# Performance work log

Hardware: AMD Instinct MI355X
Metric: run time of the kernel (lower is better)

## Reference

```python
import jax, jax.numpy as jnp
import numpy as np

WS = 32          # window_size -> N = WS*WS = 1024
DIM = 1024
HEADS = 16
BATCH = 16


def _local_mask():
    # token i maps to grid cell (i//WS, i%WS); attend iff within 3x3 neighborhood
    idx = jnp.arange(WS * WS)
    r, c = idx // WS, idx % WS
    return (jnp.abs(r[:, None] - r[None, :]) <= 1) & (jnp.abs(c[:, None] - c[None, :]) <= 1)


def setup_inputs() -> dict:
    key = jax.random.key(0)
    k1, k2, k3 = jax.random.split(key, 3)
    N = WS * WS
    x = jax.random.normal(k1, (BATCH, N, DIM), dtype=jnp.float32)
    w_qkv = jax.random.normal(k2, (3 * DIM, DIM), dtype=jnp.float32) * 0.02
    w_proj = jax.random.normal(k3, (DIM, DIM), dtype=jnp.float32) * 0.02
    b_proj = jnp.zeros((DIM,), dtype=jnp.float32)
    return {"x": x, "w_qkv": w_qkv, "w_proj": w_proj, "b_proj": b_proj}


def reference(x, w_qkv, w_proj, b_proj):
    B, N, C = x.shape
    H = HEADS
    D = C // H
    scale = D ** (-0.5)
    # qkv projection: torch Linear is x @ W^T
    qkv = (x @ w_qkv.T).reshape(B, N, 3, H, D).transpose(2, 0, 3, 1, 4)  # (3,B,H,N,D)
    q, k, v = qkv[0], qkv[1], qkv[2]
    attn = jnp.einsum('bhnd,bhmd->bhnm', q, k) * scale  # (B,H,N,N)
    mask = _local_mask()  # (N,N) bool
    attn = jnp.where(mask[None, None], attn, -jnp.inf)
    attn = jax.nn.softmax(attn, axis=-1)
    out = jnp.einsum('bhnm,bhmd->bhnd', attn, v)          # (B,H,N,D)
    out = out.transpose(0, 2, 1, 3).reshape(B, N, C)      # (B,N,C)
    return out @ w_proj.T + b_proj
```

## Files before the change

### kernel.cpp

```cpp
#include <hip/hip_runtime.h>
#include <hip/hip_bf16.h>
#include <stdint.h>


typedef __bf16 bf16;
typedef __bf16 bf16x4_t __attribute__((ext_vector_type(4)));
typedef __bf16 bf16x8_t __attribute__((ext_vector_type(8)));
typedef float f32x4_t __attribute__((ext_vector_type(4)));

static __device__ __forceinline__ void gload_lds16(const void* g, void* l) {
  __builtin_amdgcn_global_load_lds((__attribute__((address_space(1))) void*)g,
                                   (__attribute__((address_space(3))) void*)l,
                                   16, 0, 0);
}

static __device__ __forceinline__ void block_barrier() {
  asm volatile("" ::: "memory");
  __builtin_amdgcn_s_barrier();
  asm volatile("" ::: "memory");
}

__global__ void cvt_all(const float* __restrict__ x, const float* __restrict__ wq,
                        const float* __restrict__ wp, bf16* __restrict__ xb,
                        bf16* __restrict__ wqb, bf16* __restrict__ wpb) {
  constexpr int NX = 4194304, NWQ = 786432;
  int i = blockIdx.x * blockDim.x + threadIdx.x;
  const float* src; bf16* dst; int off;
  if (i < NX)            { src = x;  dst = xb;  off = i; }
  else if (i < NX + NWQ) { src = wq; dst = wqb; off = i - NX; }
  else                   { src = wp; dst = wpb; off = i - (NX + NWQ); }
  float4 v = reinterpret_cast<const float4*>(src)[off];
  bf16x4_t o;
  o[0] = (bf16)v.x; o[1] = (bf16)v.y; o[2] = (bf16)v.z; o[3] = (bf16)v.w;
  reinterpret_cast<bf16x4_t*>(dst)[off] = o;
}

template<int OUT_BF16>
__global__ __launch_bounds__(512, 2)
void gemm3s(const bf16* __restrict__ A, const bf16* __restrict__ Bm,
            void* __restrict__ Cout, const float* __restrict__ bias,
            int M, int N, int K) {
  constexpr int SLOT = 32768;
  extern __shared__ __align__(16) char lds[];

  const int tid = threadIdx.x;
  const int w = tid >> 6, lane = tid & 63;
  const int fr = lane & 15, g = lane >> 4;
  const int wr = w >> 2, wc = w & 3;

  const int nwg = gridDim.x * gridDim.y;
  int lid = blockIdx.y * gridDim.x + blockIdx.x;
  lid = (lid & 7) * (nwg >> 3) + (lid >> 3);
  const int bx = lid % gridDim.x, by = lid / gridDim.x;
  const int row0 = by * 256, col0 = bx * 256;

  const bf16* Ag = A + (size_t)row0 * K;
  const bf16* Bg = Bm + (size_t)col0 * K;
  const int srow = tid >> 2;
  const int scol = ((tid & 3) ^ ((tid >> 3) & 3)) * 8;
  const int nkt  = K >> 5;

  f32x4_t acc[8][4] = {};

  auto stage = [&](int kt, int slot) {
    const int kb = kt << 5;
    char* sb = lds + slot * SLOT;
    gload_lds16(Ag + (size_t)(srow) * K + kb + scol,       sb + tid * 16);
    gload_lds16(Ag + (size_t)(128 + srow) * K + kb + scol, sb + 8192 + tid * 16);
    gload_lds16(Bg + (size_t)(srow) * K + kb + scol,       sb + 16384 + tid * 16);
    gload_lds16(Bg + (size_t)(128 + srow) * K + kb + scol, sb + 24576 + tid * 16);
  };

  const int uxor = ((fr >> 1) & 3) << 4;

  stage(0, 0);
  stage(1, 1);
  asm volatile("s_waitcnt vmcnt(4)" ::: "memory");
  block_barrier();

  int sl = 0;
  for (int kt = 0; kt < nkt; ++kt) {
    const bool pf = (kt + 2 < nkt);
    int s2 = sl + 2; if (s2 >= 3) s2 -= 3;
    if (pf) stage(kt + 2, s2);
    const char* cA = lds + sl * SLOT;
    const char* cB = cA + 16384;

    bf16x8_t a0[4], a1[4], b0[2], b1[2];
    auto lda = [&](bf16x8_t (&dst)[4], int q) {
#pragma unroll
      for (int i = 0; i < 4; ++i) {
        const int row = wr * 128 + (q * 4 + i) * 16 + fr;
        dst[i] = *reinterpret_cast<const bf16x8_t*>(cA + (row << 6) + ((g << 4) ^ uxor));
      }
    };
    auto ldb = [&](bf16x8_t (&dst)[2], int q) {
#pragma unroll
      for (int j = 0; j < 2; ++j) {
        const int row = wc * 64 + (q * 2 + j) * 16 + fr;
        dst[j] = *reinterpret_cast<const bf16x8_t*>(cB + (row << 6) + ((g << 4) ^ uxor));
      }
    };

    lda(a0, 0);
    ldb(b0, 0);
#pragma unroll
    for (int i = 0; i < 4; ++i)
#pragma unroll
      for (int j = 0; j < 2; ++j)
        acc[i][j] = __builtin_amdgcn_mfma_f32_16x16x32_bf16(a0[i], b0[j], acc[i][j], 0, 0, 0);
    ldb(b1, 1);
#pragma unroll
    for (int i = 0; i < 4; ++i)
#pragma unroll
      for (int j = 0; j < 2; ++j)
        acc[i][2 + j] = __builtin_amdgcn_mfma_f32_16x16x32_bf16(a0[i], b1[j], acc[i][2 + j], 0, 0, 0);
    lda(a1, 1);
#pragma unroll
    for (int i = 0; i < 4; ++i)
#pragma unroll
      for (int j = 0; j < 2; ++j)
        acc[4 + i][2 + j] = __builtin_amdgcn_mfma_f32_16x16x32_bf16(
            a1[i], b1[j], acc[4 + i][2 + j], 0, 0, 0);
#pragma unroll
    for (int i = 0; i < 4; ++i)
#pragma unroll
      for (int j = 0; j < 2; ++j)
        acc[4 + i][j] = __builtin_amdgcn_mfma_f32_16x16x32_bf16(
            a1[i], b0[j], acc[4 + i][j], 0, 0, 0);

    if (pf) asm volatile("s_waitcnt vmcnt(4)" ::: "memory");
    else    asm volatile("s_waitcnt vmcnt(0)" ::: "memory");
    block_barrier();
    sl = (sl + 1 == 3) ? 0 : sl + 1;
  }

#pragma unroll
  for (int fm = 0; fm < 8; ++fm) {
    const int rbase = row0 + wr * 128 + fm * 16 + g * 4;
#pragma unroll
    for (int fn = 0; fn < 4; ++fn) {
      const int col = col0 + wc * 64 + fn * 16 + fr;
#pragma unroll
      for (int r = 0; r < 4; ++r) {
        const size_t idx = (size_t)(rbase + r) * N + col;
        if constexpr (OUT_BF16) {
          reinterpret_cast<bf16*>(Cout)[idx] = (bf16)acc[fm][fn][r];
        } else {
          reinterpret_cast<float*>(Cout)[idx] = acc[fm][fn][r] + bias[col];
        }
      }
    }
  }
}

__global__ __launch_bounds__(256)
void local_attn(const bf16* __restrict__ qkv, bf16* __restrict__ outp) {
  const int tid  = threadIdx.x;
  const int wave = tid >> 6, lane = tid & 63;
  const int tsub = lane >> 3, ch = lane & 7;
  const int gt = (blockIdx.x * 4 + wave) * 8 + tsub;
  const int i  = gt & 1023;
  const int bh = gt >> 10;
  const int h  = bh & 15, b = bh >> 4;
  const int r  = i >> 5, c = i & 31;

  const bf16* base = qkv + (size_t)(b * 1024) * 3072 + h * 64 + ch * 8;

  bf16x8_t qv = *reinterpret_cast<const bf16x8_t*>(base + (size_t)i * 3072);
  float qf[8];
#pragma unroll
  for (int e = 0; e < 8; ++e) qf[e] = (float)qv[e];

  int jj[9]; float inval[9];
#pragma unroll
  for (int t = 0; t < 9; ++t) {
    const int dr = t / 3 - 1, dc = t % 3 - 1;
    const int rr = r + dr, cc = c + dc;
    const int rcl = min(max(rr, 0), 31), ccl = min(max(cc, 0), 31);
    jj[t] = rcl * 32 + ccl;
    inval[t] = (rr == rcl && cc == ccl) ? 0.f : -1e30f;
  }

  bf16x8_t kv[9], vv[9];
#pragma unroll
  for (int t = 0; t < 9; ++t)
    kv[t] = *reinterpret_cast<const bf16x8_t*>(base + (size_t)jj[t] * 3072 + 1024);
#pragma unroll
  for (int t = 0; t < 9; ++t)
    vv[t] = *reinterpret_cast<const bf16x8_t*>(base + (size_t)jj[t] * 3072 + 2048);

  float s[9];
#pragma unroll
  for (int t = 0; t < 9; ++t) {
    float ps = 0.f;
#pragma unroll
    for (int e = 0; e < 8; ++e) ps += qf[e] * (float)kv[t][e];
    ps += __shfl_xor(ps, 1);
    ps += __shfl_xor(ps, 2);
    ps += __shfl_xor(ps, 4);
    s[t] = ps * 0.125f + inval[t];
  }

  float mx = s[0];
#pragma unroll
  for (int t = 1; t < 9; ++t) mx = fmaxf(mx, s[t]);

  float denom = 0.f, o[8] = {};
#pragma unroll
  for (int t = 0; t < 9; ++t) {
    const float p = __expf(s[t] - mx);
    denom += p;
#pragma unroll
    for (int e = 0; e < 8; ++e) o[e] += p * (float)vv[t][e];
  }

  const float inv = 1.f / denom;
  bf16x8_t ov;
#pragma unroll
  for (int e = 0; e < 8; ++e) ov[e] = (bf16)(o[e] * inv);
  *reinterpret_cast<bf16x8_t*>(outp + (size_t)(b * 1024 + i) * 1024 + h * 64 + ch * 8) = ov;
}

extern "C" void kernel_launch(void* const* d_in, const int* in_sizes, int n_in,
                              void* d_out, int out_size, void* d_ws, size_t ws_size,
                              hipStream_t stream) {
  const float* x      = (const float*)d_in[0];
  const float* w_qkv  = (const float*)d_in[1];
  const float* w_proj = (const float*)d_in[2];
  const float* b_proj = (const float*)d_in[3];
  float* out = (float*)d_out;

  const size_t nx   = (size_t)16384 * 1024;
  const size_t nwq  = (size_t)3072 * 1024;
  const size_t nwp  = (size_t)1024 * 1024;
  const size_t nqkv = (size_t)16384 * 3072;

  bf16* x_bf  = (bf16*)d_ws;
  bf16* wq_bf = x_bf + nx;
  bf16* wp_bf = wq_bf + nwq;
  bf16* qkv   = wp_bf + nwp;
  bf16* attn  = qkv + nqkv;

  (void)hipFuncSetAttribute((const void*)&gemm3s<1>,
                            hipFuncAttributeMaxDynamicSharedMemorySize, 98304);
  (void)hipFuncSetAttribute((const void*)&gemm3s<0>,
                            hipFuncAttributeMaxDynamicSharedMemorySize, 98304);

  cvt_all<<<20480, 256, 0, stream>>>(x, w_qkv, w_proj, x_bf, wq_bf, wp_bf);

  gemm3s<1><<<dim3(3072 / 256, 16384 / 256), 512, 98304, stream>>>(
      x_bf, wq_bf, qkv, nullptr, 16384, 3072, 1024);

  local_attn<<<8192, 256, 0, stream>>>(qkv, attn);

  gemm3s<0><<<dim3(1024 / 256, 16384 / 256), 512, 98304, stream>>>(
      attn, wp_bf, out, b_proj, 16384, 1024, 1024);
}
```

Baseline: 213.0 us.

## Shrink GEMM tile to 256x128 with 4 waves and stage attention K/V rows in LDS

The GEMM drops from 256x256 tiles with 8 waves to 256x128 tiles with 4 waves, which shrinks LDS per stage and doubles the number of workgroups. The goal is better occupancy and load balance across CUs. The local attention kernel now maps one block to one (batch, head, row). It loads the three neighbouring K/V token rows into LDS once, so each token no longer issues 9 separate global gathers. In exchange, each GEMM tile reuses less data, and the attention kernel adds a barrier and LDS traffic.

```diff
diff --git a/kernel.cpp b/kernel.cpp
--- a/kernel.cpp
+++ b/kernel.cpp
@@ -36,23 +36,23 @@
 }
 
 template<int OUT_BF16>
-__global__ __launch_bounds__(512, 2)
-void gemm3s(const bf16* __restrict__ A, const bf16* __restrict__ Bm,
+__global__ __launch_bounds__(256, 2)
+void gemm4w(const bf16* __restrict__ A, const bf16* __restrict__ Bm,
             void* __restrict__ Cout, const float* __restrict__ bias,
             int M, int N, int K) {
-  constexpr int SLOT = 32768;
+  constexpr int SLOT = 24576;
   extern __shared__ __align__(16) char lds[];
 
   const int tid = threadIdx.x;
   const int w = tid >> 6, lane = tid & 63;
   const int fr = lane & 15, g = lane >> 4;
-  const int wr = w >> 2, wc = w & 3;
+  const int wr = w >> 1, wc = w & 1;
 
   const int nwg = gridDim.x * gridDim.y;
   int lid = blockIdx.y * gridDim.x + blockIdx.x;
   lid = (lid & 7) * (nwg >> 3) + (lid >> 3);
   const int bx = lid % gridDim.x, by = lid / gridDim.x;
-  const int row0 = by * 256, col0 = bx * 256;
+  const int row0 = by * 256, col0 = bx * 128;
 
   const bf16* Ag = A + (size_t)row0 * K;
   const bf16* Bg = Bm + (size_t)col0 * K;
@@ -65,17 +65,21 @@
   auto stage = [&](int kt, int slot) {
     const int kb = kt << 5;
     char* sb = lds + slot * SLOT;
-    gload_lds16(Ag + (size_t)(srow) * K + kb + scol,       sb + tid * 16);
-    gload_lds16(Ag + (size_t)(128 + srow) * K + kb + scol, sb + 8192 + tid * 16);
-    gload_lds16(Bg + (size_t)(srow) * K + kb + scol,       sb + 16384 + tid * 16);
-    gload_lds16(Bg + (size_t)(128 + srow) * K + kb + scol, sb + 24576 + tid * 16);
+#pragma unroll
+    for (int n = 0; n < 4; ++n)
+      gload_lds16(Ag + (size_t)(n * 64 + srow) * K + kb + scol,
+                  sb + n * 4096 + tid * 16);
+#pragma unroll
+    for (int n = 0; n < 2; ++n)
+      gload_lds16(Bg + (size_t)(n * 64 + srow) * K + kb + scol,
+                  sb + 16384 + n * 4096 + tid * 16);
   };
 
   const int uxor = ((fr >> 1) & 3) << 4;
 
   stage(0, 0);
   stage(1, 1);
-  asm volatile("s_waitcnt vmcnt(4)" ::: "memory");
+  asm volatile("s_waitcnt vmcnt(6)" ::: "memory");
   block_barrier();
 
   int sl = 0;
@@ -129,7 +133,7 @@
         acc[4 + i][j] = __builtin_amdgcn_mfma_f32_16x16x32_bf16(
             a1[i], b0[j], acc[4 + i][j], 0, 0, 0);
 
-    if (pf) asm volatile("s_waitcnt vmcnt(4)" ::: "memory");
+    if (pf) asm volatile("s_waitcnt vmcnt(6)" ::: "memory");
     else    asm volatile("s_waitcnt vmcnt(0)" ::: "memory");
     block_barrier();
     sl = (sl + 1 == 3) ? 0 : sl + 1;
@@ -156,50 +160,55 @@
 
 __global__ __launch_bounds__(256)
 void local_attn(const bf16* __restrict__ qkv, bf16* __restrict__ outp) {
+  __shared__ __align__(16) char sK[12288];
+  __shared__ __align__(16) char sV[12288];
+
   const int tid  = threadIdx.x;
-  const int wave = tid >> 6, lane = tid & 63;
-  const int tsub = lane >> 3, ch = lane & 7;
-  const int gt = (blockIdx.x * 4 + wave) * 8 + tsub;
-  const int i  = gt & 1023;
-  const int bh = gt >> 10;
-  const int h  = bh & 15, b = bh >> 4;
-  const int r  = i >> 5, c = i & 31;
-
-  const bf16* base = qkv + (size_t)(b * 1024) * 3072 + h * 64 + ch * 8;
-
-  bf16x8_t qv = *reinterpret_cast<const bf16x8_t*>(base + (size_t)i * 3072);
+  const int w = tid >> 6, lane = tid & 63;
+  const int ch = lane & 7;
+  const int bid = blockIdx.x;
+  const int r = bid & 31, h = (bid >> 5) & 15, b = bid >> 9;
+
+  const bf16* qkvb = qkv + (size_t)(b * 1024) * 3072 + h * 64;
+  const int tokp = w * 8 + (lane >> 3);
+
+#pragma unroll
+  for (int u = 0; u < 3; ++u) {
+    const int jrow = min(max(r - 1 + u, 0), 31);
+    const size_t j = (size_t)(jrow * 32 + tokp);
+    gload_lds16(qkvb + j * 3072 + 1024 + ch * 8, sK + u * 4096 + w * 1024 + (lane & 7) * 16 + (lane >> 3) * 128);
+  }
+#pragma unroll
+  for (int u = 0; u < 3; ++u) {
+    const int jrow = min(max(r - 1 + u, 0), 31);
+    const size_t j = (size_t)(jrow * 32 + tokp);
+    gload_lds16(qkvb + j * 3072 + 2048 + ch * 8, sV + u * 4096 + w * 1024 + (lane & 7) * 16 + (lane >> 3) * 128);
+  }
+
+  const int c = tokp, i = r * 32 + c;
+  bf16x8_t qv = *reinterpret_cast<const bf16x8_t*>(qkvb + (size_t)i * 3072 + ch * 8);
   float qf[8];
 #pragma unroll
   for (int e = 0; e < 8; ++e) qf[e] = (float)qv[e];
 
-  int jj[9]; float inval[9];
+  __syncthreads();
+
+  float s[9];
 #pragma unroll
   for (int t = 0; t < 9; ++t) {
     const int dr = t / 3 - 1, dc = t % 3 - 1;
     const int rr = r + dr, cc = c + dc;
-    const int rcl = min(max(rr, 0), 31), ccl = min(max(cc, 0), 31);
-    jj[t] = rcl * 32 + ccl;
-    inval[t] = (rr == rcl && cc == ccl) ? 0.f : -1e30f;
-  }
-
-  bf16x8_t kv[9], vv[9];
-#pragma unroll
-  for (int t = 0; t < 9; ++t)
-    kv[t] = *reinterpret_cast<const bf16x8_t*>(base + (size_t)jj[t] * 3072 + 1024);
-#pragma unroll
-  for (int t = 0; t < 9; ++t)
-    vv[t] = *reinterpret_cast<const bf16x8_t*>(base + (size_t)jj[t] * 3072 + 2048);
-
-  float s[9];
-#pragma unroll
-  for (int t = 0; t < 9; ++t) {
+    const int ccl = min(max(cc, 0), 31);
+    const int wtok = (dr + 1) * 32 + ccl;
+    const bf16x8_t kvv = *reinterpret_cast<const bf16x8_t*>(sK + wtok * 128 + ch * 16);
     float ps = 0.f;
 #pragma unroll
-    for (int e = 0; e < 8; ++e) ps += qf[e] * (float)kv[t][e];
+    for (int e = 0; e < 8; ++e) ps += qf[e] * (float)kvv[e];
     ps += __shfl_xor(ps, 1);
     ps += __shfl_xor(ps, 2);
     ps += __shfl_xor(ps, 4);
-    s[t] = ps * 0.125f + inval[t];
+    const bool valid = (rr >= 0 && rr < 32 && cc >= 0 && cc < 32);
+    s[t] = ps * 0.125f + (valid ? 0.f : -1e30f);
   }
 
   float mx = s[0];
@@ -209,10 +218,14 @@
   float denom = 0.f, o[8] = {};
 #pragma unroll
   for (int t = 0; t < 9; ++t) {
+    const int dr = t / 3 - 1, dc = t % 3 - 1;
+    const int ccl = min(max(c + dc, 0), 31);
+    const int wtok = (dr + 1) * 32 + ccl;
     const float p = __expf(s[t] - mx);
     denom += p;
-#pragma unroll
-    for (int e = 0; e < 8; ++e) o[e] += p * (float)vv[t][e];
+    const bf16x8_t vvv = *reinterpret_cast<const bf16x8_t*>(sV + wtok * 128 + ch * 16);
+#pragma unroll
+    for (int e = 0; e < 8; ++e) o[e] += p * (float)vvv[e];
   }
 
   const float inv = 1.f / denom;
@@ -242,18 +255,18 @@
   bf16* qkv   = wp_bf + nwp;
   bf16* attn  = qkv + nqkv;
 
-  (void)hipFuncSetAttribute((const void*)&gemm3s<1>,
-                            hipFuncAttributeMaxDynamicSharedMemorySize, 98304);
-  (void)hipFuncSetAttribute((const void*)&gemm3s<0>,
-                            hipFuncAttributeMaxDynamicSharedMemorySize, 98304);
+  (void)hipFuncSetAttribute((const void*)&gemm4w<1>,
+                            hipFuncAttributeMaxDynamicSharedMemorySize, 73728);
+  (void)hipFuncSetAttribute((const void*)&gemm4w<0>,
+                            hipFuncAttributeMaxDynamicSharedMemorySize, 73728);
 
   cvt_all<<<20480, 256, 0, stream>>>(x, w_qkv, w_proj, x_bf, wq_bf, wp_bf);
 
-  gemm3s<1><<<dim3(3072 / 256, 16384 / 256), 512, 98304, stream>>>(
+  gemm4w<1><<<dim3(3072 / 128, 16384 / 256), 256, 73728, stream>>>(
       x_bf, wq_bf, qkv, nullptr, 16384, 3072, 1024);
 
   local_attn<<<8192, 256, 0, stream>>>(qkv, attn);
 
-  gemm3s<0><<<dim3(1024 / 256, 16384 / 256), 512, 98304, stream>>>(
+  gemm4w<0><<<dim3(1024 / 128, 16384 / 256), 256, 73728, stream>>>(
       attn, wp_bf, out, b_proj, 16384, 1024, 1024);
 }
```

Result: no change. 212.8 us (-0.1%).
